# Kernel optimization log

Measured on AMD Instinct MI355X. Metric: run time of the kernel, lower is better.

## Reference

```python
import jax, jax.numpy as jnp
import numpy as np

N_NODES = 100000
N_EDGES = 1600000
D_IN = 128
D_HID = 128
N_LAYERS = 3


def setup_inputs() -> dict:
    key = jax.random.key(0)
    ks = jax.random.split(key, 7)
    x = jax.random.normal(ks[0], (N_NODES, D_IN), dtype=jnp.float32)
    edge_index = jax.random.randint(ks[1], (2, N_EDGES), 0, N_NODES, dtype=jnp.int32)
    s = 1.0 / np.sqrt(D_HID)
    # stacked per-layer MLP params: lin1 (in->h), lin2 (h->h); in==h==128 for all layers
    W1 = jax.random.uniform(ks[2], (N_LAYERS, D_IN, D_HID), jnp.float32, -s, s)
    b1 = jax.random.uniform(ks[3], (N_LAYERS, D_HID), jnp.float32, -s, s)
    W2 = jax.random.uniform(ks[4], (N_LAYERS, D_HID, D_HID), jnp.float32, -s, s)
    b2 = jax.random.uniform(ks[5], (N_LAYERS, D_HID), jnp.float32, -s, s)
    return {"x": x, "edge_index": edge_index, "W1": W1, "b1": b1, "W2": W2, "b2": b2}


def _gin_layer(x, src, dst, W1, b1, W2, b2):
    # GINConv: out = MLP((1+eps)*x + sum_{j in N(i)} x_j), eps = 0
    agg = jax.ops.segment_sum(x[src], dst, num_segments=N_NODES)  # [N, C]
    h = x + agg
    h = jnp.maximum(h @ W1 + b1, 0.0)  # MLP internal ReLU
    return h @ W2 + b2


def reference(x, edge_index, W1, b1, W2, b2):
    src, dst = edge_index[0], edge_index[1]
    for i in range(N_LAYERS):
        x = _gin_layer(x, src, dst, W1[i], b1[i], W2[i], b2[i])
        if i < N_LAYERS - 1:  # inter-layer act (norm=Identity, dropout=0)
            x = jnp.maximum(x, 0.0)
    return x
```

## Files before the change

kernel.cpp:

```cpp
#include <hip/hip_runtime.h>
#include <hip/hip_bf16.h>

#define D 128

typedef float f32x4 __attribute__((ext_vector_type(4)));
typedef __bf16 bf16x8 __attribute__((ext_vector_type(8)));

__device__ __forceinline__ unsigned short f2bf(float f) {
  unsigned int u = __float_as_uint(f);
  u += 0x7fff + ((u >> 16) & 1);
  return (unsigned short)(u >> 16);
}

__device__ __forceinline__ void gl_lds16(const void* g, void* l) {
  __builtin_amdgcn_global_load_lds(
      (const __attribute__((address_space(1))) unsigned int*)g,
      (__attribute__((address_space(3))) unsigned int*)l, 16, 0, 0);
}

__device__ __forceinline__ int wave_incl_scan(int v, int lane) {
#pragma unroll
  for (int d = 1; d < 64; d <<= 1) {
    int t = __shfl_up(v, d);
    if (lane >= d) v += t;
  }
  return v;
}

#define NBK 196
#define CHUNK 4096

__global__ __launch_bounds__(256) void k_bhist(const int* __restrict__ dst, int E,
                                               int* __restrict__ bcount) {
  __shared__ int cnt[NBK];
  const int tid = threadIdx.x;
  for (int i = tid; i < NBK; i += 256) cnt[i] = 0;
  __syncthreads();
  const int e0 = blockIdx.x * CHUNK;
  const int emax = min(e0 + CHUNK, E);
  for (int e = e0 + tid; e < emax; e += 256)
    atomicAdd(&cnt[((unsigned)dst[e]) >> 9], 1);
  __syncthreads();
  for (int i = tid; i < NBK; i += 256)
    if (cnt[i]) atomicAdd(&bcount[i], cnt[i]);
}

__global__ void k_bscan(const int* __restrict__ bcount, int* __restrict__ bucket_base) {
  int t = threadIdx.x;
  int lane = t & 63, w = t >> 6;
  int v = (t < NBK) ? bcount[t] : 0;
  int s = wave_incl_scan(v, lane);
  __shared__ int ws[4];
  if (lane == 63) ws[w] = s;
  __syncthreads();
  int off = 0;
  for (int i = 0; i < w; i++) off += ws[i];
  if (t < NBK) bucket_base[t] = off + s - v;
  if (t == 0) bucket_base[NBK] = ws[0] + ws[1] + ws[2] + ws[3];
}

__global__ __launch_bounds__(256) void k_binA(const int* __restrict__ src,
                                              const int* __restrict__ dst, int E,
                                              const int* __restrict__ bucket_base,
                                              int* __restrict__ bcursor,
                                              int* __restrict__ pairbuf) {
  __shared__ int cnt[NBK];
  __shared__ int base[NBK];
  const int tid = threadIdx.x;
  const int e0 = blockIdx.x * CHUNK;
  const int emax = min(e0 + CHUNK, E);
  for (int i = tid; i < NBK; i += 256) cnt[i] = 0;
  __syncthreads();
  for (int e = e0 + tid; e < emax; e += 256)
    atomicAdd(&cnt[((unsigned)dst[e]) >> 9], 1);
  __syncthreads();
  for (int i = tid; i < NBK; i += 256) {
    int c = cnt[i];
    int b = 0;
    if (c) b = atomicAdd(&bcursor[i], c) + bucket_base[i];
    base[i] = b;
    cnt[i] = 0;
  }
  __syncthreads();
  for (int e = e0 + tid; e < emax; e += 256) {
    int d = dst[e];
    int bk = ((unsigned)d) >> 9;
    int pos = base[bk] + atomicAdd(&cnt[bk], 1);
    pairbuf[pos] = (src[e] << 9) | (d & 511);
  }
}

#define SEG_CAP 12800
__global__ __launch_bounds__(256) void k_binB(const int* __restrict__ pairbuf,
                                              const int* __restrict__ bucket_base,
                                              int* __restrict__ col,
                                              int* __restrict__ row_ptr, int N) {
  __shared__ int sdeg[512];
  __shared__ int rpl[512];
  __shared__ int cur[512];
  __shared__ int wsum[4];
  __shared__ int stage[SEG_CAP];
  const int tid = threadIdx.x;
  const int lane = tid & 63, wid = tid >> 6;
  const int node0 = blockIdx.x << 9;
  const int nn = min(512, N - node0);
  const int start = bucket_base[blockIdx.x];
  const int end = bucket_base[blockIdx.x + 1];
  const int sz = end - start;
  for (int i = tid; i < 512; i += 256) { sdeg[i] = 0; cur[i] = 0; }
  __syncthreads();
  for (int i = tid; i < sz; i += 256)
    atomicAdd(&sdeg[pairbuf[start + i] & 511], 1);
  __syncthreads();
  int a = sdeg[2 * tid], b = sdeg[2 * tid + 1];
  int v = a + b;
  int s = wave_incl_scan(v, lane);
  if (lane == 63) wsum[wid] = s;
  __syncthreads();
  int off = 0;
  for (int k = 0; k < wid; k++) off += wsum[k];
  int e0l = off + s - v;
  rpl[2 * tid] = e0l;
  rpl[2 * tid + 1] = e0l + a;
  __syncthreads();
  for (int i = tid; i < nn; i += 256) row_ptr[node0 + i] = start + rpl[i];
  if (blockIdx.x == gridDim.x - 1 && tid == 0) row_ptr[N] = end;
  for (int i = tid; i < sz; i += 256) {
    int pk = pairbuf[start + i];
    int d = pk & 511;
    int pos = rpl[d] + atomicAdd(&cur[d], 1);
    if (pos < SEG_CAP) stage[pos] = (int)(((unsigned)pk) >> 9);
  }
  __syncthreads();
  for (int i = tid; i < sz; i += 256) col[start + i] = stage[i];
}

#define ISSUE8(vv, cvh, base)                              \
  _Pragma("unroll") for (int u = 0; u < 8; u++) {          \
    int s_ = __shfl((cvh), (base) + u);                    \
    vv[u] = Yu[(size_t)s_ * 64 + lane];                    \
  }

#define REDUCE8(vv, jb)                                    \
  _Pragma("unroll") for (int u = 0; u < 8; u++) {          \
    float fx_ = __uint_as_float(vv[u] << 16);              \
    float fy_ = __uint_as_float(vv[u] & 0xffff0000u);      \
    if ((jb) + u < degA) { axA += fx_; ayA += fy_; }       \
    else { axB += fx_; ayB += fy_; }                       \
  }

__global__ __launch_bounds__(256) void k_agg(const unsigned short* __restrict__ Y,
                                             const int* __restrict__ row_ptr,
                                             const int* __restrict__ col,
                                             const float* __restrict__ bias,
                                             unsigned short* __restrict__ H, int N) {
  const int pw = (blockIdx.x * 256 + threadIdx.x) >> 6;
  const int lane = threadIdx.x & 63;
  const int nA = pw * 2, nB = nA + 1;
  if (nA >= N) return;
  const bool hasB = (nB < N);
  const unsigned int* Yu = (const unsigned int*)Y;
  unsigned int svA = Yu[(size_t)nA * 64 + lane];
  unsigned int svB = hasB ? Yu[(size_t)nB * 64 + lane] : 0u;
  float2 bv = ((const float2*)bias)[lane];
  int rsA = row_ptr[nA];
  int reA = row_ptr[nA + 1];
  int reB = hasB ? row_ptr[nA + 2] : reA;
  rsA = __builtin_amdgcn_readfirstlane(rsA);
  reA = __builtin_amdgcn_readfirstlane(reA);
  reB = __builtin_amdgcn_readfirstlane(reB);
  const int degA = min(reA - rsA, 64);
  const int degB = min(reB - reA, 64);
  const int m = degA + degB;
  const int mPad = (m + 7) & ~7;
  const int nb = mPad >> 3;

  float axA = bv.x + __uint_as_float(svA << 16);
  float ayA = bv.y + __uint_as_float(svA & 0xffff0000u);
  float axB = bv.x + __uint_as_float(svB << 16);
  float ayB = bv.y + __uint_as_float(svB & 0xffff0000u);

  int cv0 = N, cv1 = N;
  if (lane < degA) cv0 = col[rsA + lane];
  else if (lane - degA < degB) cv0 = col[reA + (lane - degA)];
  if (64 + lane < m) cv1 = col[reA + (64 + lane - degA)];

  unsigned int b0[8], b1[8];
  int issued = 0, done = 0;
  if (nb > 0) { ISSUE8(b0, cv0, 0); issued = 1; }
  if (nb > 1) { ISSUE8(b1, cv0, 8); issued = 2; }
  while (done < nb) {
    if ((done & 1) == 0) { REDUCE8(b0, (done << 3)); }
    else { REDUCE8(b1, (done << 3)); }
    done++;
    if (issued < nb) {
      int ch = (issued < 8) ? cv0 : cv1;
      int bs = (issued & 7) << 3;
      if ((issued & 1) == 0) { ISSUE8(b0, ch, bs); }
      else { ISSUE8(b1, ch, bs); }
      issued++;
    }
  }
  for (int t = rsA + 64; t < reA; t++) {
    unsigned int v = Yu[(size_t)col[t] * 64 + lane];
    axA += __uint_as_float(v << 16);
    ayA += __uint_as_float(v & 0xffff0000u);
  }
  for (int t = reA + 64; t < reB; t++) {
    unsigned int v = Yu[(size_t)col[t] * 64 + lane];
    axB += __uint_as_float(v << 16);
    ayB += __uint_as_float(v & 0xffff0000u);
  }

  unsigned int pA = ((unsigned int)f2bf(fmaxf(ayA, 0.f)) << 16) | f2bf(fmaxf(axA, 0.f));
  ((unsigned int*)H)[(size_t)nA * 64 + lane] = pA;
  if (hasB) {
    unsigned int pB = ((unsigned int)f2bf(fmaxf(ayB, 0.f)) << 16) | f2bf(fmaxf(axB, 0.f));
    ((unsigned int*)H)[(size_t)nB * 64 + lane] = pB;
  }
}

__global__ void k_prep(const float* __restrict__ W1, const float* __restrict__ W2,
                       unsigned short* __restrict__ Wt) {
  int b = blockIdx.x;
  const float* W = (b & 1) ? (W2 + (size_t)(b >> 1) * D * D) : (W1 + (size_t)(b >> 1) * D * D);
  unsigned short* O = Wt + (size_t)b * D * D;
  for (int i = threadIdx.x; i < D * D; i += 256) {
    int n = i >> 7, k = i & 127;
    O[n * D + k] = f2bf(W[k * D + n]);
  }
}

template <bool A_FP32, bool OUT_FP32>
__global__ __launch_bounds__(256) void k_gemm(const void* __restrict__ Ain,
                                              const unsigned short* __restrict__ Wt,
                                              const float* __restrict__ bias,
                                              void* __restrict__ Cout, int M, int relu) {
  __shared__ __align__(16) unsigned short As[64 * 128];
  __shared__ __align__(16) unsigned short Bs[128 * 128];
  const int tid = threadIdx.x;
  const int wid = tid >> 6, lane = tid & 63;
  const int R0 = blockIdx.x * 64;

#pragma unroll
  for (int g = 0; g < 8; g++) {
    int flat = g * 256 + tid;
    int n = flat >> 4, p = flat & 15;
    int l = p ^ (n & 15);
    gl_lds16(Wt + (size_t)n * D + l * 8, &Bs[(size_t)(g * 256 + wid * 64) * 8]);
  }
  if (A_FP32) {
    const float* A = (const float*)Ain;
#pragma unroll
    for (int g = 0; g < 4; g++) {
      int flat = g * 256 + tid;
      int row = flat >> 4, p = flat & 15;
      int l = p ^ (row & 15);
      float4 a0 = make_float4(0.f, 0.f, 0.f, 0.f), a1 = a0;
      if (R0 + row < M) {
        a0 = *(const float4*)(A + (size_t)(R0 + row) * D + l * 8);
        a1 = *(const float4*)(A + (size_t)(R0 + row) * D + l * 8 + 4);
      }
      ushort4 v0, v1;
      v0.x = f2bf(a0.x); v0.y = f2bf(a0.y); v0.z = f2bf(a0.z); v0.w = f2bf(a0.w);
      v1.x = f2bf(a1.x); v1.y = f2bf(a1.y); v1.z = f2bf(a1.z); v1.w = f2bf(a1.w);
      *(ushort4*)&As[row * D + p * 8] = v0;
      *(ushort4*)&As[row * D + p * 8 + 4] = v1;
    }
  } else {
    const unsigned short* A = (const unsigned short*)Ain;
#pragma unroll
    for (int g = 0; g < 4; g++) {
      int flat = g * 256 + tid;
      int row = flat >> 4, p = flat & 15;
      int l = p ^ (row & 15);
      gl_lds16(A + (size_t)(R0 + row) * D + l * 8, &As[(size_t)(g * 256 + wid * 64) * 8]);
    }
  }
  __syncthreads();

  const int wr = wid >> 1, wc = wid & 1;
  const int lm = lane & 15, lq = lane >> 4;
  f32x4 acc[2][4];
#pragma unroll
  for (int i = 0; i < 2; i++)
#pragma unroll
    for (int j = 0; j < 4; j++) acc[i][j] = f32x4{0.f, 0.f, 0.f, 0.f};

#pragma unroll
  for (int kc = 0; kc < 4; kc++) {
    const int pc = (kc * 4 + lq) ^ lm;
    bf16x8 af[2], bfr[4];
#pragma unroll
    for (int i = 0; i < 2; i++)
      af[i] = *(const bf16x8*)&As[(wr * 32 + i * 16 + lm) * D + pc * 8];
#pragma unroll
    for (int j = 0; j < 4; j++)
      bfr[j] = *(const bf16x8*)&Bs[(wc * 64 + j * 16 + lm) * D + pc * 8];
#pragma unroll
    for (int i = 0; i < 2; i++)
#pragma unroll
      for (int j = 0; j < 4; j++)
        acc[i][j] = __builtin_amdgcn_mfma_f32_16x16x32_bf16(af[i], bfr[j], acc[i][j], 0, 0, 0);
  }

  float bv[4];
#pragma unroll
  for (int j = 0; j < 4; j++) bv[j] = bias ? bias[wc * 64 + j * 16 + lm] : 0.f;
#pragma unroll
  for (int i = 0; i < 2; i++) {
#pragma unroll
    for (int reg = 0; reg < 4; reg++) {
      const int gr = R0 + wr * 32 + i * 16 + lq * 4 + reg;
      if (gr < M) {
#pragma unroll
        for (int j = 0; j < 4; j++) {
          const int gc = wc * 64 + j * 16 + lm;
          float v = acc[i][j][reg] + bv[j];
          if (relu) v = fmaxf(v, 0.f);
          if (OUT_FP32)
            ((float*)Cout)[(size_t)gr * D + gc] = v;
          else
            ((unsigned short*)Cout)[(size_t)gr * D + gc] = f2bf(v);
        }
      }
    }
  }
}

__global__ __launch_bounds__(256) void k_gemm2(const unsigned short* __restrict__ Ain,
                                               const unsigned short* __restrict__ W2t,
                                               const unsigned short* __restrict__ W1t,
                                               const float* __restrict__ b2,
                                               unsigned short* __restrict__ Cout, int M) {
  __shared__ __align__(16) unsigned short As[64 * 128];
  __shared__ __align__(16) unsigned short Bs[128 * 128];
  const int tid = threadIdx.x;
  const int wid = tid >> 6, lane = tid & 63;
  const int R0 = blockIdx.x * 64;

#pragma unroll
  for (int g = 0; g < 8; g++) {
    int flat = g * 256 + tid;
    int n = flat >> 4, p = flat & 15;
    int l = p ^ (n & 15);
    gl_lds16(W2t + (size_t)n * D + l * 8, &Bs[(size_t)(g * 256 + wid * 64) * 8]);
  }
#pragma unroll
  for (int g = 0; g < 4; g++) {
    int flat = g * 256 + tid;
    int row = flat >> 4, p = flat & 15;
    int l = p ^ (row & 15);
    gl_lds16(Ain + (size_t)(R0 + row) * D + l * 8, &As[(size_t)(g * 256 + wid * 64) * 8]);
  }
  __syncthreads();

  const int wr = wid >> 1, wc = wid & 1;
  const int lm = lane & 15, lq = lane >> 4;
  f32x4 acc[2][4];
#pragma unroll
  for (int i = 0; i < 2; i++)
#pragma unroll
    for (int j = 0; j < 4; j++) acc[i][j] = f32x4{0.f, 0.f, 0.f, 0.f};
#pragma unroll
  for (int kc = 0; kc < 4; kc++) {
    const int pc = (kc * 4 + lq) ^ lm;
    bf16x8 af[2], bfr[4];
#pragma unroll
    for (int i = 0; i < 2; i++)
      af[i] = *(const bf16x8*)&As[(wr * 32 + i * 16 + lm) * D + pc * 8];
#pragma unroll
    for (int j = 0; j < 4; j++)
      bfr[j] = *(const bf16x8*)&Bs[(wc * 64 + j * 16 + lm) * D + pc * 8];
#pragma unroll
    for (int i = 0; i < 2; i++)
#pragma unroll
      for (int j = 0; j < 4; j++)
        acc[i][j] = __builtin_amdgcn_mfma_f32_16x16x32_bf16(af[i], bfr[j], acc[i][j], 0, 0, 0);
  }
  __syncthreads();

#pragma unroll
  for (int g = 0; g < 8; g++) {
    int flat = g * 256 + tid;
    int n = flat >> 4, p = flat & 15;
    int l = p ^ (n & 15);
    gl_lds16(W1t + (size_t)n * D + l * 8, &Bs[(size_t)(g * 256 + wid * 64) * 8]);
  }
  {
    float bv[4];
#pragma unroll
    for (int j = 0; j < 4; j++) bv[j] = b2[wc * 64 + j * 16 + lm];
#pragma unroll
    for (int i = 0; i < 2; i++) {
#pragma unroll
      for (int reg = 0; reg < 4; reg++) {
        const int row = wr * 32 + i * 16 + lq * 4 + reg;
#pragma unroll
        for (int j = 0; j < 4; j++) {
          const int gc = wc * 64 + j * 16 + lm;
          float v = fmaxf(acc[i][j][reg] + bv[j], 0.f);
          As[row * D + (((gc >> 3) ^ (row & 15)) << 3) + (gc & 7)] = f2bf(v);
        }
      }
    }
  }
  __syncthreads();

  f32x4 acc2[2][4];
#pragma unroll
  for (int i = 0; i < 2; i++)
#pragma unroll
    for (int j = 0; j < 4; j++) acc2[i][j] = f32x4{0.f, 0.f, 0.f, 0.f};
#pragma unroll
  for (int kc = 0; kc < 4; kc++) {
    const int pc = (kc * 4 + lq) ^ lm;
    bf16x8 af[2], bfr[4];
#pragma unroll
    for (int i = 0; i < 2; i++)
      af[i] = *(const bf16x8*)&As[(wr * 32 + i * 16 + lm) * D + pc * 8];
#pragma unroll
    for (int j = 0; j < 4; j++)
      bfr[j] = *(const bf16x8*)&Bs[(wc * 64 + j * 16 + lm) * D + pc * 8];
#pragma unroll
    for (int i = 0; i < 2; i++)
#pragma unroll
      for (int j = 0; j < 4; j++)
        acc2[i][j] = __builtin_amdgcn_mfma_f32_16x16x32_bf16(af[i], bfr[j], acc2[i][j], 0, 0, 0);
  }
#pragma unroll
  for (int i = 0; i < 2; i++) {
#pragma unroll
    for (int reg = 0; reg < 4; reg++) {
      const int gr = R0 + wr * 32 + i * 16 + lq * 4 + reg;
      if (gr < M) {
#pragma unroll
        for (int j = 0; j < 4; j++) {
          const int gc = wc * 64 + j * 16 + lm;
          Cout[(size_t)gr * D + gc] = f2bf(acc2[i][j][reg]);
        }
      }
    }
  }
}

extern "C" void kernel_launch(void* const* d_in, const int* in_sizes, int n_in,
                              void* d_out, int out_size, void* d_ws, size_t ws_size,
                              hipStream_t stream) {
  const float* x  = (const float*)d_in[0];
  const int*   ei = (const int*)d_in[1];
  const float* W1 = (const float*)d_in[2];
  const float* b1 = (const float*)d_in[3];
  const float* W2 = (const float*)d_in[4];
  const float* b2 = (const float*)d_in[5];
  const int N = in_sizes[0] / D;
  const int E = in_sizes[1] / 2;
  const int* src = ei;
  const int* dst = ei + E;

  char* ws = (char*)d_ws;
  unsigned short* Wt   = (unsigned short*)ws;
  unsigned short* bufA = Wt + 6 * D * D;
  unsigned short* bufB = bufA + (size_t)(N + 1) * D;
  int* pairbuf = (int*)bufB;
  int* row_ptr = (int*)(bufB + (size_t)(N + 1) * D);
  int* colv    = row_ptr + (N + 1);
  int* bucket_base = colv + E;
  int* bcount  = bucket_base + 256;
  int* bcursor = bcount + 256;
  float* OUT   = (float*)d_out;

  const int CB = (E + CHUNK - 1) / CHUNK;
  const int GB = (N + 63) / 64;
  const int AB = ((N + 1) / 2 + 3) / 4;
  const int BKB = (N + 511) / 512;

  k_prep<<<6, 256, 0, stream>>>(W1, W2, Wt);
  hipMemsetAsync(bcount, 0, 512 * sizeof(int), stream);
  hipMemsetAsync(bufA + (size_t)N * D, 0, D * sizeof(unsigned short), stream);
  hipMemsetAsync(bufB + (size_t)N * D, 0, D * sizeof(unsigned short), stream);
  k_bhist<<<CB, 256, 0, stream>>>(dst, E, bcount);
  k_bscan<<<1, 256, 0, stream>>>(bcount, bucket_base);
  k_binA<<<CB, 256, 0, stream>>>(src, dst, E, bucket_base, bcursor, pairbuf);
  k_binB<<<BKB, 256, 0, stream>>>(pairbuf, bucket_base, colv, row_ptr, N);

  k_gemm<true, false><<<GB, 256, 0, stream>>>(x, Wt + 0 * D * D, nullptr, bufA, N, 0);
  k_agg<<<AB, 256, 0, stream>>>(bufA, row_ptr, colv, b1, bufB, N);
  k_gemm2<<<GB, 256, 0, stream>>>(bufB, Wt + 1 * D * D, Wt + 2 * D * D, b2, bufA, N);
  k_agg<<<AB, 256, 0, stream>>>(bufA, row_ptr, colv, b1 + D, bufB, N);
  k_gemm2<<<GB, 256, 0, stream>>>(bufB, Wt + 3 * D * D, Wt + 4 * D * D, b2 + D, bufA, N);
  k_agg<<<AB, 256, 0, stream>>>(bufA, row_ptr, colv, b1 + 2 * D, bufB, N);
  k_gemm<false, true><<<GB, 256, 0, stream>>>(bufB, Wt + 5 * D * D, b2 + 2 * D, OUT, N, 0);
  (void)n_in; (void)out_size; (void)ws_size;
}
```

Measured before the change: 426.9 us.

## Drop bucket scan kernel and memsets; simplify aggregation to one node per wave

The standalone bucket-scan kernel is removed. Each binning block now recomputes the bucket prefix from the raw counts, and the count reset moves into the weight-prep kernel, which cuts three memsets and one launch. The aggregation kernel goes back from two nodes per wave with a double-buffered gather pipeline to one node per wave with batches of eight loads. This shortens the launch chain but may lose memory-level parallelism in the dominant gather kernel, and the padding-row memsets are dropped.

```diff
diff --git a/kernel.cpp b/kernel.cpp
--- a/kernel.cpp
+++ b/kernel.cpp
@@ -45,31 +45,31 @@
     if (cnt[i]) atomicAdd(&bcount[i], cnt[i]);
 }
 
-__global__ void k_bscan(const int* __restrict__ bcount, int* __restrict__ bucket_base) {
-  int t = threadIdx.x;
-  int lane = t & 63, w = t >> 6;
-  int v = (t < NBK) ? bcount[t] : 0;
-  int s = wave_incl_scan(v, lane);
-  __shared__ int ws[4];
-  if (lane == 63) ws[w] = s;
-  __syncthreads();
-  int off = 0;
-  for (int i = 0; i < w; i++) off += ws[i];
-  if (t < NBK) bucket_base[t] = off + s - v;
-  if (t == 0) bucket_base[NBK] = ws[0] + ws[1] + ws[2] + ws[3];
-}
-
 __global__ __launch_bounds__(256) void k_binA(const int* __restrict__ src,
                                               const int* __restrict__ dst, int E,
-                                              const int* __restrict__ bucket_base,
+                                              const int* __restrict__ bcount,
                                               int* __restrict__ bcursor,
                                               int* __restrict__ pairbuf) {
   __shared__ int cnt[NBK];
   __shared__ int base[NBK];
+  __shared__ int bb[NBK];
+  __shared__ int ws4[4];
   const int tid = threadIdx.x;
   const int e0 = blockIdx.x * CHUNK;
   const int emax = min(e0 + CHUNK, E);
   for (int i = tid; i < NBK; i += 256) cnt[i] = 0;
+  {
+    int lane = tid & 63, w = tid >> 6;
+    int v = (tid < NBK) ? bcount[tid] : 0;
+    int s = wave_incl_scan(v, lane);
+    if (lane == 63) ws4[w] = s;
+    __syncthreads();
+    if (tid < NBK) {
+      int off = 0;
+      for (int k = 0; k < w; k++) off += ws4[k];
+      bb[tid] = off + s - v;
+    }
+  }
   __syncthreads();
   for (int e = e0 + tid; e < emax; e += 256)
     atomicAdd(&cnt[((unsigned)dst[e]) >> 9], 1);
@@ -77,7 +77,7 @@
   for (int i = tid; i < NBK; i += 256) {
     int c = cnt[i];
     int b = 0;
-    if (c) b = atomicAdd(&bcursor[i], c) + bucket_base[i];
+    if (c) b = atomicAdd(&bcursor[i], c) + bb[i];
     base[i] = b;
     cnt[i] = 0;
   }
@@ -92,23 +92,31 @@
 
 #define SEG_CAP 12800
 __global__ __launch_bounds__(256) void k_binB(const int* __restrict__ pairbuf,
-                                              const int* __restrict__ bucket_base,
+                                              const int* __restrict__ bcount,
                                               int* __restrict__ col,
                                               int* __restrict__ row_ptr, int N) {
   __shared__ int sdeg[512];
   __shared__ int rpl[512];
   __shared__ int cur[512];
   __shared__ int wsum[4];
+  __shared__ int wsum2[4];
   __shared__ int stage[SEG_CAP];
   const int tid = threadIdx.x;
   const int lane = tid & 63, wid = tid >> 6;
   const int node0 = blockIdx.x << 9;
   const int nn = min(512, N - node0);
-  const int start = bucket_base[blockIdx.x];
-  const int end = bucket_base[blockIdx.x + 1];
+  {
+    int vv = (tid < (int)blockIdx.x) ? bcount[tid] : 0;
+    vv += __shfl_down(vv, 32); vv += __shfl_down(vv, 16);
+    vv += __shfl_down(vv, 8);  vv += __shfl_down(vv, 4);
+    vv += __shfl_down(vv, 2);  vv += __shfl_down(vv, 1);
+    if (lane == 0) wsum2[wid] = vv;
+  }
+  for (int i = tid; i < 512; i += 256) { sdeg[i] = 0; cur[i] = 0; }
+  __syncthreads();
+  const int start = wsum2[0] + wsum2[1] + wsum2[2] + wsum2[3];
+  const int end = start + bcount[blockIdx.x];
   const int sz = end - start;
-  for (int i = tid; i < 512; i += 256) { sdeg[i] = 0; cur[i] = 0; }
-  __syncthreads();
   for (int i = tid; i < sz; i += 256)
     atomicAdd(&sdeg[pairbuf[start + i] & 511], 1);
   __syncthreads();
@@ -135,100 +143,76 @@
   for (int i = tid; i < sz; i += 256) col[start + i] = stage[i];
 }
 
-#define ISSUE8(vv, cvh, base)                              \
-  _Pragma("unroll") for (int u = 0; u < 8; u++) {          \
-    int s_ = __shfl((cvh), (base) + u);                    \
-    vv[u] = Yu[(size_t)s_ * 64 + lane];                    \
-  }
-
-#define REDUCE8(vv, jb)                                    \
-  _Pragma("unroll") for (int u = 0; u < 8; u++) {          \
-    float fx_ = __uint_as_float(vv[u] << 16);              \
-    float fy_ = __uint_as_float(vv[u] & 0xffff0000u);      \
-    if ((jb) + u < degA) { axA += fx_; ayA += fy_; }       \
-    else { axB += fx_; ayB += fy_; }                       \
-  }
+__global__ void k_prep(const float* __restrict__ W1, const float* __restrict__ W2,
+                       unsigned short* __restrict__ Wt, int* __restrict__ bcount) {
+  int b = blockIdx.x;
+  if (b < 6) {
+    const float* W = (b & 1) ? (W2 + (size_t)(b >> 1) * D * D) : (W1 + (size_t)(b >> 1) * D * D);
+    unsigned short* O = Wt + (size_t)b * D * D;
+    for (int i = threadIdx.x; i < D * D; i += 256) {
+      int n = i >> 7, k = i & 127;
+      O[n * D + k] = f2bf(W[k * D + n]);
+    }
+  } else {
+    for (int i = threadIdx.x; i < 512; i += 256) bcount[i] = 0;
+  }
+}
 
 __global__ __launch_bounds__(256) void k_agg(const unsigned short* __restrict__ Y,
                                              const int* __restrict__ row_ptr,
                                              const int* __restrict__ col,
                                              const float* __restrict__ bias,
                                              unsigned short* __restrict__ H, int N) {
-  const int pw = (blockIdx.x * 256 + threadIdx.x) >> 6;
-  const int lane = threadIdx.x & 63;
-  const int nA = pw * 2, nB = nA + 1;
-  if (nA >= N) return;
-  const bool hasB = (nB < N);
+  int wid = (blockIdx.x * 256 + threadIdx.x) >> 6;
+  int lane = threadIdx.x & 63;
+  if (wid >= N) return;
   const unsigned int* Yu = (const unsigned int*)Y;
-  unsigned int svA = Yu[(size_t)nA * 64 + lane];
-  unsigned int svB = hasB ? Yu[(size_t)nB * 64 + lane] : 0u;
+  unsigned int sv = Yu[(size_t)wid * 64 + lane];
   float2 bv = ((const float2*)bias)[lane];
-  int rsA = row_ptr[nA];
-  int reA = row_ptr[nA + 1];
-  int reB = hasB ? row_ptr[nA + 2] : reA;
-  rsA = __builtin_amdgcn_readfirstlane(rsA);
-  reA = __builtin_amdgcn_readfirstlane(reA);
-  reB = __builtin_amdgcn_readfirstlane(reB);
-  const int degA = min(reA - rsA, 64);
-  const int degB = min(reB - reA, 64);
-  const int m = degA + degB;
-  const int mPad = (m + 7) & ~7;
-  const int nb = mPad >> 3;
-
-  float axA = bv.x + __uint_as_float(svA << 16);
-  float ayA = bv.y + __uint_as_float(svA & 0xffff0000u);
-  float axB = bv.x + __uint_as_float(svB << 16);
-  float ayB = bv.y + __uint_as_float(svB & 0xffff0000u);
-
-  int cv0 = N, cv1 = N;
-  if (lane < degA) cv0 = col[rsA + lane];
-  else if (lane - degA < degB) cv0 = col[reA + (lane - degA)];
-  if (64 + lane < m) cv1 = col[reA + (64 + lane - degA)];
-
-  unsigned int b0[8], b1[8];
-  int issued = 0, done = 0;
-  if (nb > 0) { ISSUE8(b0, cv0, 0); issued = 1; }
-  if (nb > 1) { ISSUE8(b1, cv0, 8); issued = 2; }
-  while (done < nb) {
-    if ((done & 1) == 0) { REDUCE8(b0, (done << 3)); }
-    else { REDUCE8(b1, (done << 3)); }
-    done++;
-    if (issued < nb) {
-      int ch = (issued < 8) ? cv0 : cv1;
-      int bs = (issued & 7) << 3;
-      if ((issued & 1) == 0) { ISSUE8(b0, ch, bs); }
-      else { ISSUE8(b1, ch, bs); }
-      issued++;
-    }
-  }
-  for (int t = rsA + 64; t < reA; t++) {
+  float ax = bv.x + __uint_as_float(sv << 16);
+  float ay = bv.y + __uint_as_float(sv & 0xffff0000u);
+  int rs = row_ptr[wid], re = row_ptr[wid + 1];
+  int deg = re - rs;
+  int dcap = min(deg, 64);
+  int cv = (lane < dcap) ? col[rs + lane] : 0;
+  int j = 0;
+  for (; j + 8 <= dcap; j += 8) {
+    int s0 = __shfl(cv, j + 0), s1 = __shfl(cv, j + 1);
+    int s2 = __shfl(cv, j + 2), s3 = __shfl(cv, j + 3);
+    int s4 = __shfl(cv, j + 4), s5 = __shfl(cv, j + 5);
+    int s6 = __shfl(cv, j + 6), s7 = __shfl(cv, j + 7);
+    unsigned int v0 = Yu[(size_t)s0 * 64 + lane];
+    unsigned int v1 = Yu[(size_t)s1 * 64 + lane];
+    unsigned int v2 = Yu[(size_t)s2 * 64 + lane];
+    unsigned int v3 = Yu[(size_t)s3 * 64 + lane];
+    unsigned int v4 = Yu[(size_t)s4 * 64 + lane];
+    unsigned int v5 = Yu[(size_t)s5 * 64 + lane];
+    unsigned int v6 = Yu[(size_t)s6 * 64 + lane];
+    unsigned int v7 = Yu[(size_t)s7 * 64 + lane];
+    ax += ((__uint_as_float(v0 << 16) + __uint_as_float(v1 << 16)) +
+           (__uint_as_float(v2 << 16) + __uint_as_float(v3 << 16))) +
+          ((__uint_as_float(v4 << 16) + __uint_as_float(v5 << 16)) +
+           (__uint_as_float(v6 << 16) + __uint_as_float(v7 << 16)));
+    ay += ((__uint_as_float(v0 & 0xffff0000u) + __uint_as_float(v1 & 0xffff0000u)) +
+           (__uint_as_float(v2 & 0xffff0000u) + __uint_as_float(v3 & 0xffff0000u))) +
+          ((__uint_as_float(v4 & 0xffff0000u) + __uint_as_float(v5 & 0xffff0000u)) +
+           (__uint_as_float(v6 & 0xffff0000u) + __uint_as_float(v7 & 0xffff0000u)));
+  }
+  for (; j < dcap; j++) {
+    int s = __shfl(cv, j);
+    unsigned int v = Yu[(size_t)s * 64 + lane];
+    ax += __uint_as_float(v << 16);
+    ay += __uint_as_float(v & 0xffff0000u);
+  }
+  for (int t = rs + 64; t < re; t++) {
     unsigned int v = Yu[(size_t)col[t] * 64 + lane];
-    axA += __uint_as_float(v << 16);
-    ayA += __uint_as_float(v & 0xffff0000u);
-  }
-  for (int t = reA + 64; t < reB; t++) {
-    unsigned int v = Yu[(size_t)col[t] * 64 + lane];
-    axB += __uint_as_float(v << 16);
-    ayB += __uint_as_float(v & 0xffff0000u);
-  }
-
-  unsigned int pA = ((unsigned int)f2bf(fmaxf(ayA, 0.f)) << 16) | f2bf(fmaxf(axA, 0.f));
-  ((unsigned int*)H)[(size_t)nA * 64 + lane] = pA;
-  if (hasB) {
-    unsigned int pB = ((unsigned int)f2bf(fmaxf(ayB, 0.f)) << 16) | f2bf(fmaxf(axB, 0.f));
-    ((unsigned int*)H)[(size_t)nB * 64 + lane] = pB;
-  }
-}
-
-__global__ void k_prep(const float* __restrict__ W1, const float* __restrict__ W2,
-                       unsigned short* __restrict__ Wt) {
-  int b = blockIdx.x;
-  const float* W = (b & 1) ? (W2 + (size_t)(b >> 1) * D * D) : (W1 + (size_t)(b >> 1) * D * D);
-  unsigned short* O = Wt + (size_t)b * D * D;
-  for (int i = threadIdx.x; i < D * D; i += 256) {
-    int n = i >> 7, k = i & 127;
-    O[n * D + k] = f2bf(W[k * D + n]);
-  }
+    ax += __uint_as_float(v << 16);
+    ay += __uint_as_float(v & 0xffff0000u);
+  }
+  ax = fmaxf(ax, 0.f);
+  ay = fmaxf(ay, 0.f);
+  unsigned int packed = ((unsigned int)f2bf(ay) << 16) | f2bf(ax);
+  ((unsigned int*)H)[(size_t)wid * 64 + lane] = packed;
 }
 
 template <bool A_FP32, bool OUT_FP32>
@@ -465,24 +449,19 @@
   int* pairbuf = (int*)bufB;
   int* row_ptr = (int*)(bufB + (size_t)(N + 1) * D);
   int* colv    = row_ptr + (N + 1);
-  int* bucket_base = colv + E;
-  int* bcount  = bucket_base + 256;
+  int* bcount  = colv + E;
   int* bcursor = bcount + 256;
   float* OUT   = (float*)d_out;
 
   const int CB = (E + CHUNK - 1) / CHUNK;
   const int GB = (N + 63) / 64;
-  const int AB = ((N + 1) / 2 + 3) / 4;
+  const int AB = (N + 3) / 4;
   const int BKB = (N + 511) / 512;
 
-  k_prep<<<6, 256, 0, stream>>>(W1, W2, Wt);
-  hipMemsetAsync(bcount, 0, 512 * sizeof(int), stream);
-  hipMemsetAsync(bufA + (size_t)N * D, 0, D * sizeof(unsigned short), stream);
-  hipMemsetAsync(bufB + (size_t)N * D, 0, D * sizeof(unsigned short), stream);
+  k_prep<<<7, 256, 0, stream>>>(W1, W2, Wt, bcount);
   k_bhist<<<CB, 256, 0, stream>>>(dst, E, bcount);
-  k_bscan<<<1, 256, 0, stream>>>(bcount, bucket_base);
-  k_binA<<<CB, 256, 0, stream>>>(src, dst, E, bucket_base, bcursor, pairbuf);
-  k_binB<<<BKB, 256, 0, stream>>>(pairbuf, bucket_base, colv, row_ptr, N);
+  k_binA<<<CB, 256, 0, stream>>>(src, dst, E, bcount, bcursor, pairbuf);
+  k_binB<<<BKB, 256, 0, stream>>>(pairbuf, bcount, colv, row_ptr, N);
 
   k_gemm<true, false><<<GB, 256, 0, stream>>>(x, Wt + 0 * D * D, nullptr, bufA, N, 0);
   k_agg<<<AB, 256, 0, stream>>>(bufA, row_ptr, colv, b1, bufB, N);
```

New measurement: 420.6 us. No clear change (-1.5%).
